# Performance work log

Measured on AMD Instinct MI355X. Metric: run time of the kernel, lower is better.

Reference implementation:

```python
import jax, jax.numpy as jnp
import numpy as np

D_MODEL, D_K, D_V, NUM_HEADS = 1024, 64, 64, 16
B, T = 4, 2048


def setup_inputs() -> dict:
    key = jax.random.key(0)
    ks = jax.random.split(key, 9)
    s = 0.02
    inp = {
        "input_Q": jax.random.normal(ks[0], (B, T, D_MODEL), dtype=jnp.float32),
        # causal mask: True = masked out (matches torch masked_fill semantics)
        "mask": jnp.triu(jnp.ones((T, T), dtype=bool), k=1),
        "Wq": jax.random.normal(ks[1], (D_MODEL, D_K * NUM_HEADS), dtype=jnp.float32) * s,
        "bq": jnp.zeros((D_K * NUM_HEADS,), dtype=jnp.float32),
        "Wk": jax.random.normal(ks[2], (D_MODEL, D_K * NUM_HEADS), dtype=jnp.float32) * s,
        "bk": jnp.zeros((D_K * NUM_HEADS,), dtype=jnp.float32),
        "Wv": jax.random.normal(ks[3], (D_MODEL, D_V * NUM_HEADS), dtype=jnp.float32) * s,
        "bv": jnp.zeros((D_V * NUM_HEADS,), dtype=jnp.float32),
        "Wo": jax.random.normal(ks[4], (D_V * NUM_HEADS, D_MODEL), dtype=jnp.float32) * s,
        "bo": jnp.zeros((D_MODEL,), dtype=jnp.float32),
    }
    return inp


def reference(input_Q, mask, Wq, bq, Wk, bk, Wv, bv, Wo, bo):
    b, t, _ = input_Q.shape
    h, dk, dv = NUM_HEADS, D_K, D_V
    # projections, then split heads: [b, t, h*d] -> [b, h, t, d]
    Q = (input_Q @ Wq + bq).reshape(b, t, h, dk).transpose(0, 2, 1, 3)
    K = (input_Q @ Wk + bk).reshape(b, t, h, dk).transpose(0, 2, 1, 3)
    V = (input_Q @ Wv + bv).reshape(b, t, h, dv).transpose(0, 2, 1, 3)
    # scaled dot-product attention with full [b, h, t, t] scores (as original)
    scores = jnp.einsum("bhqd,bhkd->bhqk", Q, K) * (1.0 / np.sqrt(dk).astype(np.float32))
    scores = jnp.where(mask, jnp.float32(-jnp.inf), scores)
    attn = jax.nn.softmax(scores, axis=-1)
    ctx = jnp.einsum("bhqk,bhkd->bhqd", attn, V)  # [b, h, t, dv]
    combined = ctx.transpose(0, 2, 1, 3).reshape(b, t, h * dv)
    return combined @ Wo + bo
```

## Files before the change

kernel.cpp:

```cpp
#include <hip/hip_runtime.h>
#include <hip/hip_bf16.h>
#include <stdint.h>

#define B_  4
#define T_  2048
#define H_  16
#define DH  64
#define DM  1024

typedef unsigned short u16;
typedef float  f32x4  __attribute__((ext_vector_type(4)));
typedef u16    u16x4  __attribute__((ext_vector_type(4)));
typedef __bf16 bf16x8 __attribute__((ext_vector_type(8)));
typedef bf16x8 __attribute__((may_alias, aligned(16))) bf16x8_a;
typedef u16x4  __attribute__((may_alias, aligned(8)))  u16x4_a;

__device__ __forceinline__ void gld16(void* lds, const void* g) {
  __builtin_amdgcn_global_load_lds((const __attribute__((address_space(1))) unsigned int*)g,
                                   (__attribute__((address_space(3))) unsigned int*)lds,
                                   16, 0, 0);
}
__device__ __forceinline__ u16 f2b(float f) {
  __bf16 h = (__bf16)f; return __builtin_bit_cast(unsigned short, h);
}

__global__ void prep(const float* __restrict__ X,
                     const float* __restrict__ Wq, const float* __restrict__ Wk,
                     const float* __restrict__ Wv, const float* __restrict__ Wo,
                     u16* __restrict__ Xb,
                     u16* __restrict__ WqT, u16* __restrict__ WkT,
                     u16* __restrict__ WvT, u16* __restrict__ WoT) {
  if (blockIdx.z == 4) {
    const int bi = blockIdx.y * 32 + blockIdx.x;
#pragma unroll
    for (int p = 0; p < 8; ++p) {
      const int i = bi * 8192 + p * 1024 + threadIdx.x * 4;
      const f32x4 v = *(const f32x4*)&X[i];
      u16x4 o;
      o.x = f2b(v.x); o.y = f2b(v.y); o.z = f2b(v.z); o.w = f2b(v.w);
      *(u16x4_a*)&Xb[i] = o;
    }
    return;
  }
  const float* in; u16* out;
  switch (blockIdx.z) {
    case 0: in = Wq; out = WqT; break;
    case 1: in = Wk; out = WkT; break;
    case 2: in = Wv; out = WvT; break;
    default: in = Wo; out = WoT; break;
  }
  __shared__ u16 t[32][33];
  const int bx = blockIdx.x * 32, by = blockIdx.y * 32;
  const int tx = threadIdx.x & 31, ty = threadIdx.x >> 5;
  for (int i = ty; i < 32; i += 8) t[i][tx] = f2b(in[(size_t)(by + i) * DM + bx + tx]);
  __syncthreads();
  for (int i = ty; i < 32; i += 8) out[(size_t)(bx + i) * DM + by + tx] = t[tx][i];
}

__global__ void transpose_v(const u16* __restrict__ in, u16* __restrict__ out) {
  __shared__ u16 t[64][65];
  const int bh = blockIdx.y, t0 = blockIdx.x * 64;
  const int tx = threadIdx.x & 63, ty = threadIdx.x >> 6;
  const u16* ib = in  + (size_t)bh * T_ * DH;
  u16*       ob = out + (size_t)bh * DH * T_;
  for (int i = ty; i < 64; i += 4) t[i][tx] = ib[(size_t)(t0 + i) * DH + tx];
  __syncthreads();
  for (int i = ty; i < 64; i += 4) ob[(size_t)i * T_ + t0 + tx] = t[tx][i];
}

__device__ __forceinline__ void gemm_bt_128(
    const u16* __restrict__ A, const u16* __restrict__ BT,
    const float* __restrict__ bias, float oscale,
    u16* __restrict__ C, float* __restrict__ Cf, int mode)
{
  constexpr int K = 1024, N = 1024;
  __shared__ __attribute__((aligned(16))) u16 lA[128 * 64];
  __shared__ __attribute__((aligned(16))) u16 lB[128 * 64];
  const int tid  = threadIdx.x;
  const int lane = tid & 63;
  const int quad = lane >> 4, ln = lane & 15;
  const int ln7 = ln & 7;
  const int wave = tid >> 6;
  const int wm = wave >> 1, wn = wave & 1;
  const int m0 = blockIdx.y * 128, n0 = blockIdx.x * 128;

  const f32x4 fz = {0.f, 0.f, 0.f, 0.f};
  f32x4 acc[4][4];
#pragma unroll
  for (int i = 0; i < 4; i++)
#pragma unroll
    for (int j = 0; j < 4; j++) acc[i][j] = fz;

  for (int k0 = 0; k0 < K; k0 += 64) {
    __syncthreads();
#pragma unroll
    for (int p = 0; p < 4; ++p) {
      const int P = p * 256 + tid;
      const int row = P >> 3, c = (P & 7) ^ (row & 7);
      gld16(&lA[P * 8], &A [(size_t)(m0 + row) * K + k0 + c * 8]);
      gld16(&lB[P * 8], &BT[(size_t)(n0 + row) * K + k0 + c * 8]);
    }
    __syncthreads();
#pragma unroll
    for (int ks = 0; ks < 2; ++ks) {
      bf16x8 af[4], bf[4];
#pragma unroll
      for (int i = 0; i < 4; i++)
        af[i] = *(const bf16x8_a*)&lA[(wm * 64 + i * 16 + ln) * 64 + (((ks * 4 + quad) ^ ln7) << 3)];
#pragma unroll
      for (int j = 0; j < 4; j++)
        bf[j] = *(const bf16x8_a*)&lB[(wn * 64 + j * 16 + ln) * 64 + (((ks * 4 + quad) ^ ln7) << 3)];
#pragma unroll
      for (int i = 0; i < 4; i++)
#pragma unroll
        for (int j = 0; j < 4; j++)
          acc[i][j] = __builtin_amdgcn_mfma_f32_16x16x32_bf16(af[i], bf[j], acc[i][j], 0, 0, 0);
    }
  }

#pragma unroll
  for (int j = 0; j < 4; j++) {
    const int n = n0 + wn * 64 + j * 16 + ln;
    const float bn = bias[n];
#pragma unroll
    for (int i = 0; i < 4; i++) {
      const int mb = m0 + wm * 64 + i * 16 + quad * 4;
#pragma unroll
      for (int r = 0; r < 4; r++) {
        const int m = mb + r;
        const float v = (acc[i][j][r] + bn) * oscale;
        if (mode == 0) {
          const int b = m >> 11, t = m & 2047, h = n >> 6, d = n & 63;
          C[((size_t)((b * H_ + h) * T_ + t)) * DH + d] = f2b(v);
        } else {
          Cf[(size_t)m * N + n] = v;
        }
      }
    }
  }
}

__global__ __launch_bounds__(256, 2) void qkv_gemm(
    const u16* __restrict__ X,
    const u16* __restrict__ WqT, const u16* __restrict__ WkT, const u16* __restrict__ WvT,
    const float* __restrict__ bq, const float* __restrict__ bk, const float* __restrict__ bv,
    u16* __restrict__ Qo, u16* __restrict__ Ko, u16* __restrict__ Vo)
{
  const u16 *BT; const float* bias; u16* C; float sc;
  if (blockIdx.z == 0)      { BT = WqT; bias = bq; C = Qo; sc = 0.1803368801111144f; }
  else if (blockIdx.z == 1) { BT = WkT; bias = bk; C = Ko; sc = 1.0f; }
  else                      { BT = WvT; bias = bv; C = Vo; sc = 1.0f; }
  gemm_bt_128(X, BT, bias, sc, C, nullptr, 0);
}

__global__ __launch_bounds__(256, 2) void out_gemm(
    const u16* __restrict__ ctx, const u16* __restrict__ WoT,
    const float* __restrict__ bo, float* __restrict__ out)
{
  gemm_bt_128(ctx, WoT, bo, 1.0f, nullptr, out, 2);
}

__global__ __launch_bounds__(512, 4) void flash_attn(
    const u16* __restrict__ Q, const u16* __restrict__ Kg,
    const u16* __restrict__ Vt, u16* __restrict__ ctx)
{
  __shared__ __attribute__((aligned(16))) u16 lK[128 * 64];
  __shared__ __attribute__((aligned(16))) u16 lV[64 * 128];
  __shared__ __attribute__((aligned(16))) u16 lP[128 * 64];

  const int bh = blockIdx.x;
  const int b  = bh >> 4, h = bh & 15;
  const int qi = 15 - blockIdx.y;
  const int q0 = qi * 128;
  const int tid = threadIdx.x;
  const int lane = tid & 63, wave = tid >> 6;
  const int quad = lane >> 4, ln = lane & 15;
  const int ln7 = ln & 7, ln8 = ln >> 3;
  const int w16 = wave * 16;

  const u16* Qbh = Q  + (size_t)bh * T_ * DH;
  const u16* Kbh = Kg + (size_t)bh * T_ * DH;
  const u16* Vbh = Vt + (size_t)bh * DH * T_;

#pragma unroll
  for (int p = 0; p < 2; ++p) {
    const int P = p * 512 + tid;
    const int row = P >> 3, c = (P & 7) ^ (row & 7);
    gld16(&lK[P * 8], &Qbh[(size_t)(q0 + row) * DH + c * 8]);
  }
  __syncthreads();
  bf16x8 aq[2];
#pragma unroll
  for (int ks = 0; ks < 2; ++ks)
    aq[ks] = *(const bf16x8_a*)&lK[(w16 + ln) * 64 + (((ks * 4 + quad) ^ ln7) << 3)];

  bf16x8 ones;
#pragma unroll
  for (int i = 0; i < 8; i++) ones[i] = (__bf16)1.0f;

  const f32x4 fz = {0.f, 0.f, 0.f, 0.f};
  f32x4 accO[4];
  f32x4 accL;
#pragma unroll
  for (int j = 0; j < 4; j++) accO[j] = fz;
  accL = fz;

  auto tile_step = [&](int kt, bool MASK) {
    const int t0 = kt * 128;
    __syncthreads();
#pragma unroll
    for (int p = 0; p < 2; ++p) {
      const int P = p * 512 + tid;
      const int row = P >> 3, c = (P & 7) ^ (row & 7);
      gld16(&lK[P * 8], &Kbh[(size_t)(t0 + row) * DH + c * 8]);
    }
#pragma unroll
    for (int p = 0; p < 2; ++p) {
      const int P = p * 512 + tid;
      const int row = P >> 4, c = (P & 15) ^ (row & 15);
      gld16(&lV[P * 8], &Vbh[(size_t)row * T_ + t0 + c * 8]);
    }
    __syncthreads();

#pragma unroll
    for (int half = 0; half < 2; ++half) {
      f32x4 s[4];
#pragma unroll
      for (int jj = 0; jj < 4; jj++) s[jj] = fz;
#pragma unroll
      for (int ks = 0; ks < 2; ++ks) {
        bf16x8 bk4[4];
#pragma unroll
        for (int jj = 0; jj < 4; jj++)
          bk4[jj] = *(const bf16x8_a*)&lK[((half * 4 + jj) * 16 + ln) * 64 + (((ks * 4 + quad) ^ ln7) << 3)];
#pragma unroll
        for (int jj = 0; jj < 4; jj++)
          s[jj] = __builtin_amdgcn_mfma_f32_16x16x32_bf16(aq[ks], bk4[jj], s[jj], 0, 0, 0);
      }

#pragma unroll
      for (int jj = 0; jj < 4; jj++)
#pragma unroll
        for (int r = 0; r < 4; r++) {
          float z = s[jj][r];
          if (MASK) {
            const int qrow = q0 + w16 + quad * 4 + r;
            if ((t0 + (half * 4 + jj) * 16 + ln) > qrow) z = -INFINITY;
          }
          s[jj][r] = __builtin_amdgcn_exp2f(z);
        }

#pragma unroll
      for (int jj = 0; jj < 4; jj++) {
        const int c = jj * 2 + ln8;
#pragma unroll
        for (int r = 0; r < 4; r++) {
          const int row = w16 + quad * 4 + r;
          lP[row * 64 + ((c ^ (row & 7)) << 3) + ln7] = f2b(s[jj][r]);
        }
      }

#pragma unroll
      for (int ks2 = 0; ks2 < 2; ++ks2) {
        const int ks = half * 2 + ks2;
        bf16x8 ap, bv4[4];
        ap = *(const bf16x8_a*)&lP[(w16 + ln) * 64 + (((ks2 * 4 + quad) ^ ln7) << 3)];
        accL = __builtin_amdgcn_mfma_f32_16x16x32_bf16(ap, ones, accL, 0, 0, 0);
#pragma unroll
        for (int j2 = 0; j2 < 4; j2++)
          bv4[j2] = *(const bf16x8_a*)&lV[(j2 * 16 + ln) * 128 + (((ks * 4 + quad) ^ ln) << 3)];
#pragma unroll
        for (int j2 = 0; j2 < 4; j2++)
          accO[j2] = __builtin_amdgcn_mfma_f32_16x16x32_bf16(ap, bv4[j2], accO[j2], 0, 0, 0);
      }
    }
  };

  for (int kt = 0; kt < qi; ++kt) tile_step(kt, false);
  tile_step(qi, true);

#pragma unroll
  for (int r = 0; r < 4; r++) {
    const int qrow = q0 + w16 + quad * 4 + r;
    const float inv = 1.0f / accL[r];
#pragma unroll
    for (int j2 = 0; j2 < 4; j2++) {
      const int d = j2 * 16 + ln;
      ctx[((size_t)(b * T_ + qrow)) * DM + h * DH + d] = f2b(accO[j2][r] * inv);
    }
  }
}

extern "C" void kernel_launch(void* const* d_in, const int* in_sizes, int n_in,
                              void* d_out, int out_size, void* d_ws, size_t ws_size,
                              hipStream_t stream) {
  (void)in_sizes; (void)n_in; (void)out_size; (void)ws_size;
  const float* X  = (const float*)d_in[0];
  const float* Wq = (const float*)d_in[2];
  const float* bq = (const float*)d_in[3];
  const float* Wk = (const float*)d_in[4];
  const float* bk = (const float*)d_in[5];
  const float* Wv = (const float*)d_in[6];
  const float* bv = (const float*)d_in[7];
  const float* Wo = (const float*)d_in[8];
  const float* bo = (const float*)d_in[9];
  float* out = (float*)d_out;

  char* ws = (char*)d_ws;
  u16* WqT = (u16*)(ws + (0ull  << 20));
  u16* WkT = (u16*)(ws + (2ull  << 20));
  u16* WvT = (u16*)(ws + (4ull  << 20));
  u16* WoT = (u16*)(ws + (6ull  << 20));
  u16* Xb  = (u16*)(ws + (8ull  << 20));
  u16* Qb  = (u16*)(ws + (24ull << 20));
  u16* Kb  = (u16*)(ws + (40ull << 20));
  u16* Vb  = (u16*)(ws + (56ull << 20));
  u16* Vtb = (u16*)(ws + (72ull << 20));
  u16* ctx = (u16*)(ws + (88ull << 20));

  prep<<<dim3(32, 32, 5), 256, 0, stream>>>(X, Wq, Wk, Wv, Wo, Xb, WqT, WkT, WvT, WoT);
  qkv_gemm<<<dim3(8, 64, 3), 256, 0, stream>>>(Xb, WqT, WkT, WvT, bq, bk, bv, Qb, Kb, Vb);
  transpose_v<<<dim3(32, 64), 256, 0, stream>>>(Vb, Vtb);
  flash_attn<<<dim3(64, 16), 512, 0, stream>>>(Qb, Kb, Vtb, ctx);
  out_gemm<<<dim3(8, 64), 256, 0, stream>>>(ctx, WoT, bo, out);
}
```

Before: 274.2 us.

## Double-buffer K/V in flash attention and fuse V transpose into QKV GEMM

Flash attention now keeps two K/V LDS buffers and prefetches the next tile with async global-to-LDS loads while the current tile is computed, waiting with partial vmcnt. It also raises wave priority around MFMA blocks. The V projection writes directly in transposed layout, which drops the separate transpose kernel and its round-trip through memory. The prep kernel switches to 64x64 transpose tiles. Costs: more LDS per block, which may reduce occupancy, and strided 2-byte stores for the V epilogue.

```diff
diff --git a/kernel.cpp b/kernel.cpp
--- a/kernel.cpp
+++ b/kernel.cpp
@@ -31,10 +31,10 @@
                      u16* __restrict__ WqT, u16* __restrict__ WkT,
                      u16* __restrict__ WvT, u16* __restrict__ WoT) {
   if (blockIdx.z == 4) {
-    const int bi = blockIdx.y * 32 + blockIdx.x;
-#pragma unroll
-    for (int p = 0; p < 8; ++p) {
-      const int i = bi * 8192 + p * 1024 + threadIdx.x * 4;
+    const int bi = blockIdx.y * 16 + blockIdx.x;
+#pragma unroll
+    for (int p = 0; p < 32; ++p) {
+      const int i = bi * 32768 + p * 1024 + threadIdx.x * 4;
       const f32x4 v = *(const f32x4*)&X[i];
       u16x4 o;
       o.x = f2b(v.x); o.y = f2b(v.y); o.z = f2b(v.z); o.w = f2b(v.w);
@@ -49,23 +49,12 @@
     case 2: in = Wv; out = WvT; break;
     default: in = Wo; out = WoT; break;
   }
-  __shared__ u16 t[32][33];
-  const int bx = blockIdx.x * 32, by = blockIdx.y * 32;
-  const int tx = threadIdx.x & 31, ty = threadIdx.x >> 5;
-  for (int i = ty; i < 32; i += 8) t[i][tx] = f2b(in[(size_t)(by + i) * DM + bx + tx]);
+  __shared__ u16 t[64][65];
+  const int bx = blockIdx.x * 64, by = blockIdx.y * 64;
+  const int tx = threadIdx.x & 63, ty = threadIdx.x >> 6;
+  for (int i = ty; i < 64; i += 4) t[i][tx] = f2b(in[(size_t)(by + i) * DM + bx + tx]);
   __syncthreads();
-  for (int i = ty; i < 32; i += 8) out[(size_t)(bx + i) * DM + by + tx] = t[tx][i];
-}
-
-__global__ void transpose_v(const u16* __restrict__ in, u16* __restrict__ out) {
-  __shared__ u16 t[64][65];
-  const int bh = blockIdx.y, t0 = blockIdx.x * 64;
-  const int tx = threadIdx.x & 63, ty = threadIdx.x >> 6;
-  const u16* ib = in  + (size_t)bh * T_ * DH;
-  u16*       ob = out + (size_t)bh * DH * T_;
-  for (int i = ty; i < 64; i += 4) t[i][tx] = ib[(size_t)(t0 + i) * DH + tx];
-  __syncthreads();
-  for (int i = ty; i < 64; i += 4) ob[(size_t)i * T_ + t0 + tx] = t[tx][i];
+  for (int i = ty; i < 64; i += 4) out[(size_t)(bx + i) * DM + by + tx] = t[tx][i];
 }
 
 __device__ __forceinline__ void gemm_bt_128(
@@ -132,6 +121,9 @@
         if (mode == 0) {
           const int b = m >> 11, t = m & 2047, h = n >> 6, d = n & 63;
           C[((size_t)((b * H_ + h) * T_ + t)) * DH + d] = f2b(v);
+        } else if (mode == 1) {
+          const int b = m >> 11, t = m & 2047, h = n >> 6, d = n & 63;
+          C[((size_t)((b * H_ + h) * DH + d)) * T_ + t] = f2b(v);
         } else {
           Cf[(size_t)m * N + n] = v;
         }
@@ -144,13 +136,13 @@
     const u16* __restrict__ X,
     const u16* __restrict__ WqT, const u16* __restrict__ WkT, const u16* __restrict__ WvT,
     const float* __restrict__ bq, const float* __restrict__ bk, const float* __restrict__ bv,
-    u16* __restrict__ Qo, u16* __restrict__ Ko, u16* __restrict__ Vo)
+    u16* __restrict__ Qo, u16* __restrict__ Ko, u16* __restrict__ Vto)
 {
-  const u16 *BT; const float* bias; u16* C; float sc;
-  if (blockIdx.z == 0)      { BT = WqT; bias = bq; C = Qo; sc = 0.1803368801111144f; }
-  else if (blockIdx.z == 1) { BT = WkT; bias = bk; C = Ko; sc = 1.0f; }
-  else                      { BT = WvT; bias = bv; C = Vo; sc = 1.0f; }
-  gemm_bt_128(X, BT, bias, sc, C, nullptr, 0);
+  const u16 *BT; const float* bias; u16* C; float sc; int mode;
+  if (blockIdx.z == 0)      { BT = WqT; bias = bq; C = Qo;  sc = 0.1803368801111144f; mode = 0; }
+  else if (blockIdx.z == 1) { BT = WkT; bias = bk; C = Ko;  sc = 1.0f;                mode = 0; }
+  else                      { BT = WvT; bias = bv; C = Vto; sc = 1.0f;                mode = 1; }
+  gemm_bt_128(X, BT, bias, sc, C, nullptr, mode);
 }
 
 __global__ __launch_bounds__(256, 2) void out_gemm(
@@ -164,8 +156,8 @@
     const u16* __restrict__ Q, const u16* __restrict__ Kg,
     const u16* __restrict__ Vt, u16* __restrict__ ctx)
 {
-  __shared__ __attribute__((aligned(16))) u16 lK[128 * 64];
-  __shared__ __attribute__((aligned(16))) u16 lV[64 * 128];
+  __shared__ __attribute__((aligned(16))) u16 lK[2][128 * 64];
+  __shared__ __attribute__((aligned(16))) u16 lV[2][64 * 128];
   __shared__ __attribute__((aligned(16))) u16 lP[128 * 64];
 
   const int bh = blockIdx.x;
@@ -182,17 +174,36 @@
   const u16* Kbh = Kg + (size_t)bh * T_ * DH;
   const u16* Vbh = Vt + (size_t)bh * DH * T_;
 
+  auto stage_kv = [&](int kt, int bufw) {
+    const int t0 = kt << 7;
+    u16* dK = lK[bufw]; u16* dV = lV[bufw];
+#pragma unroll
+    for (int p = 0; p < 2; ++p) {
+      const int P = p * 512 + tid;
+      const int row = P >> 3, c = (P & 7) ^ (row & 7);
+      gld16(&dK[P * 8], &Kbh[(size_t)(t0 + row) * DH + c * 8]);
+    }
+#pragma unroll
+    for (int p = 0; p < 2; ++p) {
+      const int P = p * 512 + tid;
+      const int row = P >> 4, c = (P & 15) ^ (row & 15);
+      gld16(&dV[P * 8], &Vbh[(size_t)row * T_ + t0 + c * 8]);
+    }
+  };
+
 #pragma unroll
   for (int p = 0; p < 2; ++p) {
     const int P = p * 512 + tid;
     const int row = P >> 3, c = (P & 7) ^ (row & 7);
-    gld16(&lK[P * 8], &Qbh[(size_t)(q0 + row) * DH + c * 8]);
-  }
-  __syncthreads();
+    gld16(&lP[P * 8], &Qbh[(size_t)(q0 + row) * DH + c * 8]);
+  }
+  stage_kv(0, 0);
+  asm volatile("s_waitcnt vmcnt(4)" ::: "memory");
+  __builtin_amdgcn_s_barrier();
   bf16x8 aq[2];
 #pragma unroll
   for (int ks = 0; ks < 2; ++ks)
-    aq[ks] = *(const bf16x8_a*)&lK[(w16 + ln) * 64 + (((ks * 4 + quad) ^ ln7) << 3)];
+    aq[ks] = *(const bf16x8_a*)&lP[(w16 + ln) * 64 + (((ks * 4 + quad) ^ ln7) << 3)];
 
   bf16x8 ones;
 #pragma unroll
@@ -205,38 +216,25 @@
   for (int j = 0; j < 4; j++) accO[j] = fz;
   accL = fz;
 
-  auto tile_step = [&](int kt, bool MASK) {
+  auto compute_tile = [&](int kt, const u16* lKb, const u16* lVb, bool MASK) {
     const int t0 = kt * 128;
-    __syncthreads();
-#pragma unroll
-    for (int p = 0; p < 2; ++p) {
-      const int P = p * 512 + tid;
-      const int row = P >> 3, c = (P & 7) ^ (row & 7);
-      gld16(&lK[P * 8], &Kbh[(size_t)(t0 + row) * DH + c * 8]);
-    }
-#pragma unroll
-    for (int p = 0; p < 2; ++p) {
-      const int P = p * 512 + tid;
-      const int row = P >> 4, c = (P & 15) ^ (row & 15);
-      gld16(&lV[P * 8], &Vbh[(size_t)row * T_ + t0 + c * 8]);
-    }
-    __syncthreads();
-
 #pragma unroll
     for (int half = 0; half < 2; ++half) {
       f32x4 s[4];
 #pragma unroll
       for (int jj = 0; jj < 4; jj++) s[jj] = fz;
+      __builtin_amdgcn_s_setprio(1);
 #pragma unroll
       for (int ks = 0; ks < 2; ++ks) {
         bf16x8 bk4[4];
 #pragma unroll
         for (int jj = 0; jj < 4; jj++)
-          bk4[jj] = *(const bf16x8_a*)&lK[((half * 4 + jj) * 16 + ln) * 64 + (((ks * 4 + quad) ^ ln7) << 3)];
+          bk4[jj] = *(const bf16x8_a*)&lKb[((half * 4 + jj) * 16 + ln) * 64 + (((ks * 4 + quad) ^ ln7) << 3)];
 #pragma unroll
         for (int jj = 0; jj < 4; jj++)
           s[jj] = __builtin_amdgcn_mfma_f32_16x16x32_bf16(aq[ks], bk4[jj], s[jj], 0, 0, 0);
       }
+      __builtin_amdgcn_s_setprio(0);
 
 #pragma unroll
       for (int jj = 0; jj < 4; jj++)
@@ -265,19 +263,32 @@
         const int ks = half * 2 + ks2;
         bf16x8 ap, bv4[4];
         ap = *(const bf16x8_a*)&lP[(w16 + ln) * 64 + (((ks2 * 4 + quad) ^ ln7) << 3)];
+#pragma unroll
+        for (int j2 = 0; j2 < 4; j2++)
+          bv4[j2] = *(const bf16x8_a*)&lVb[(j2 * 16 + ln) * 128 + (((ks * 4 + quad) ^ ln) << 3)];
+        __builtin_amdgcn_s_setprio(1);
         accL = __builtin_amdgcn_mfma_f32_16x16x32_bf16(ap, ones, accL, 0, 0, 0);
-#pragma unroll
-        for (int j2 = 0; j2 < 4; j2++)
-          bv4[j2] = *(const bf16x8_a*)&lV[(j2 * 16 + ln) * 128 + (((ks * 4 + quad) ^ ln) << 3)];
 #pragma unroll
         for (int j2 = 0; j2 < 4; j2++)
           accO[j2] = __builtin_amdgcn_mfma_f32_16x16x32_bf16(ap, bv4[j2], accO[j2], 0, 0, 0);
+        __builtin_amdgcn_s_setprio(0);
       }
     }
   };
 
-  for (int kt = 0; kt < qi; ++kt) tile_step(kt, false);
-  tile_step(qi, true);
+  int buf = 0;
+  for (int kt = 0; kt < qi; ++kt) {
+    __builtin_amdgcn_s_barrier();
+    stage_kv(kt + 1, buf ^ 1);
+    asm volatile("s_waitcnt vmcnt(4)" ::: "memory");
+    __builtin_amdgcn_s_barrier();
+    compute_tile(kt, lK[buf], lV[buf], false);
+    buf ^= 1;
+  }
+  __builtin_amdgcn_s_barrier();
+  asm volatile("s_waitcnt vmcnt(0)" ::: "memory");
+  __builtin_amdgcn_s_barrier();
+  compute_tile(qi, lK[buf], lV[buf], true);
 
 #pragma unroll
   for (int r = 0; r < 4; r++) {
@@ -314,13 +325,11 @@
   u16* Xb  = (u16*)(ws + (8ull  << 20));
   u16* Qb  = (u16*)(ws + (24ull << 20));
   u16* Kb  = (u16*)(ws + (40ull << 20));
-  u16* Vb  = (u16*)(ws + (56ull << 20));
   u16* Vtb = (u16*)(ws + (72ull << 20));
   u16* ctx = (u16*)(ws + (88ull << 20));
 
-  prep<<<dim3(32, 32, 5), 256, 0, stream>>>(X, Wq, Wk, Wv, Wo, Xb, WqT, WkT, WvT, WoT);
-  qkv_gemm<<<dim3(8, 64, 3), 256, 0, stream>>>(Xb, WqT, WkT, WvT, bq, bk, bv, Qb, Kb, Vb);
-  transpose_v<<<dim3(32, 64), 256, 0, stream>>>(Vb, Vtb);
+  prep<<<dim3(16, 16, 5), 256, 0, stream>>>(X, Wq, Wk, Wv, Wo, Xb, WqT, WkT, WvT, WoT);
+  qkv_gemm<<<dim3(8, 64, 3), 256, 0, stream>>>(Xb, WqT, WkT, WvT, bq, bk, bv, Qb, Kb, Vtb);
   flash_attn<<<dim3(64, 16), 512, 0, stream>>>(Qb, Kb, Vtb, ctx);
   out_gemm<<<dim3(8, 64), 256, 0, stream>>>(ctx, WoT, bo, out);
 }
```

Result: no change. 279.1 us (+1.8%).
